# Optimization experiments

Hardware: AMD Instinct MI355X
Metric: run time of the kernel (lower is better)

Reference implementation:

```python
import jax, jax.numpy as jnp
import numpy as np

N_NODES = 20000
LN_EPS = 1e-5


def setup_inputs() -> dict:
    key = jax.random.key(0)
    ks = jax.random.split(key, 8)
    N, E, D_IN, D_H = N_NODES, 320000, 128, 256
    x = jax.random.normal(ks[0], (N, D_IN), dtype=jnp.float32)
    edge_index = jax.random.randint(ks[1], (2, E), 0, N, dtype=jnp.int64)
    edge_weight = jax.random.uniform(ks[2], (E,), dtype=jnp.float32)
    # Glorot-ish scaled weights
    W1 = jax.random.normal(ks[3], (D_IN, D_H), dtype=jnp.float32) / np.sqrt(D_IN)
    W2 = jax.random.normal(ks[4], (D_H, D_H), dtype=jnp.float32) / np.sqrt(D_H)
    Wres = jax.random.normal(ks[5], (D_IN, D_H), dtype=jnp.float32) / np.sqrt(D_IN)
    return {
        "x": x, "edge_index": edge_index, "edge_weight": edge_weight,
        "W1": W1, "b1": jnp.zeros((D_H,), jnp.float32),
        "W2": W2, "b2": jnp.zeros((D_H,), jnp.float32),
        "Wres": Wres, "bres": jnp.zeros((D_H,), jnp.float32),
        "gamma1": jnp.ones((D_H,), jnp.float32), "beta1": jnp.zeros((D_H,), jnp.float32),
        "gamma2": jnp.ones((D_H,), jnp.float32), "beta2": jnp.zeros((D_H,), jnp.float32),
    }


def _gcn_conv(x, W, b, src, dst, w, n):
    # PyG GCNConv: linear transform, then sym-normalized scatter-add aggregation
    h = x @ W  # [N, D_H]
    deg = jax.ops.segment_sum(w, dst, num_segments=n)  # in-degree incl. self loops
    dinv = jnp.where(deg > 0, jax.lax.rsqrt(deg), 0.0)
    norm = dinv[src] * w * dinv[dst]  # [E+N]
    out = jax.ops.segment_sum(norm[:, None] * h[src], dst, num_segments=n)
    return out + b


def _layer_norm(x, gamma, beta):
    mu = jnp.mean(x, axis=-1, keepdims=True)
    var = jnp.mean(jnp.square(x - mu), axis=-1, keepdims=True)
    return (x - mu) * jax.lax.rsqrt(var + LN_EPS) * gamma + beta


def reference(x, edge_index, edge_weight, W1, b1, W2, b2, Wres, bres,
              gamma1, beta1, gamma2, beta2):
    n = x.shape[0]
    loop = jnp.arange(n, dtype=edge_index.dtype)
    # add self loops with weight 1 (add_self_loops=True)
    src = jnp.concatenate([edge_index[0], loop])
    dst = jnp.concatenate([edge_index[1], loop])
    w = jnp.concatenate([edge_weight, jnp.ones((n,), edge_weight.dtype)])

    # hop 0: conv -> relu (dropout p=0, eval) -> residual proj -> LayerNorm
    delta = jax.nn.relu(_gcn_conv(x, W1, b1, src, dst, w, n))
    h = _layer_norm(x @ Wres + bres + delta, gamma1, beta1)

    # hop 1 (last): conv -> residual -> LayerNorm (no relu)
    delta = _gcn_conv(h, W2, b2, src, dst, w, n)
    h = _layer_norm(h + delta, gamma2, beta2)
    return h
```

## Files before the change

kernel.cpp:

```cpp
#include <hip/hip_runtime.h>
#include <stdint.h>


constexpr int DIN = 128;
constexpr int DH  = 256;
#define LN_EPS 1e-5f

typedef __attribute__((ext_vector_type(8))) short bf16x8;
typedef __attribute__((ext_vector_type(4))) short bf16x4;
typedef __attribute__((ext_vector_type(4))) float f32x4;

__device__ __forceinline__ short f2bf(float f) {
  union { float f; unsigned u; } v; v.f = f;
  unsigned r = v.u + 0x7fffu + ((v.u >> 16) & 1u);
  return (short)(r >> 16);
}
__device__ __forceinline__ float bf2f(short b) {
  union { unsigned u; float f; } v; v.u = ((unsigned)(unsigned short)b) << 16;
  return v.f;
}

__device__ __forceinline__ int probe_m64(const unsigned* ei) {
  int lane = threadIdx.x & 63;
  unsigned v = ei[2 * (lane * 32) + 1];
  return __ballot(v != 0u) == 0ull;
}

__device__ __forceinline__ int eidx(const void* ei, long long e, int m64) {
  return m64 ? (int)((const long long*)ei)[e] : ((const int*)ei)[e];
}


__global__ __launch_bounds__(256) void k_prep(const float* __restrict__ x,
                                              short* __restrict__ xb,
                                              const float* __restrict__ W1,
                                              const float* __restrict__ Wres,
                                              const float* __restrict__ W2,
                                              short* __restrict__ W1t,
                                              short* __restrict__ Wrt,
                                              short* __restrict__ W2t,
                                              float* __restrict__ deg,
                                              int* __restrict__ cnt, int N) {
  const int NXV = N * DIN / 8;
  const int NW  = DIN * DH;
  const int NW2 = DH * DH;
  int idx = blockIdx.x * 256 + threadIdx.x;
  if (idx < NXV) {
    f32x4 a = ((const f32x4*)x)[idx * 2];
    f32x4 b = ((const f32x4*)x)[idx * 2 + 1];
    bf16x8 o;
    o[0] = f2bf(a[0]); o[1] = f2bf(a[1]); o[2] = f2bf(a[2]); o[3] = f2bf(a[3]);
    o[4] = f2bf(b[0]); o[5] = f2bf(b[1]); o[6] = f2bf(b[2]); o[7] = f2bf(b[3]);
    ((bf16x8*)xb)[idx] = o;
    return;
  }
  idx -= NXV;
  if (idx < N) { deg[idx] = 1.0f; cnt[idx] = 0; return; }
  idx -= N;
  if (idx < NW) {
    int n = idx / DIN, k = idx % DIN;
    W1t[idx] = f2bf(W1[k * DH + n]);
    return;
  }
  idx -= NW;
  if (idx < NW) {
    int n = idx / DIN, k = idx % DIN;
    Wrt[idx] = f2bf(Wres[k * DH + n]);
    return;
  }
  idx -= NW;
  if (idx < NW2) {
    int n = idx / DH, k = idx % DH;
    W2t[idx] = f2bf(W2[k * DH + n]);
  }
}


__global__ __launch_bounds__(256) void k_edge_accum(const void* ei,
                                                    const float* __restrict__ w,
                                                    float* deg, int* cnt, int E) {
  int m64 = probe_m64((const unsigned*)ei);
  int e = blockIdx.x * 256 + threadIdx.x;
  if (e >= E) return;
  int d = eidx(ei, (long long)E + e, m64);
  atomicAdd(&deg[d], w[e]);
  atomicAdd(&cnt[d], 1);
}


__global__ __launch_bounds__(1024) void k_scan(const int* __restrict__ cnt,
                                               float* deg, int* rowptr,
                                               int* cursor, int n) {
  for (int i = threadIdx.x; i < n; i += 1024) deg[i] = rsqrtf(deg[i]);

  __shared__ int wsum[16];
  __shared__ int carry_s;
  int tid = threadIdx.x, lane = tid & 63, wv = tid >> 6;
  if (tid == 0) { carry_s = 0; rowptr[0] = 0; cursor[0] = 0; }
  __syncthreads();
  for (int c0 = 0; c0 < n; c0 += 1024) {
    int i = c0 + tid;
    int sc = (i < n) ? cnt[i] : 0;
#pragma unroll
    for (int off = 1; off < 64; off <<= 1) {
      int t = __shfl_up(sc, off, 64);
      if (lane >= off) sc += t;
    }
    if (lane == 63) wsum[wv] = sc;
    __syncthreads();
    if (wv == 0) {
      int s = (lane < 16) ? wsum[lane] : 0;
#pragma unroll
      for (int off = 1; off < 16; off <<= 1) {
        int t = __shfl_up(s, off, 64);
        if (lane >= off) s += t;
      }
      if (lane < 16) wsum[lane] = s;
    }
    __syncthreads();
    int inc = sc + ((wv > 0) ? wsum[wv - 1] : 0) + carry_s;
    if (i < n) { rowptr[i + 1] = inc; cursor[i + 1] = inc; }
    __syncthreads();
    if (tid == 0) carry_s += wsum[15];
    __syncthreads();
  }
}


__global__ __launch_bounds__(256) void k_fill(const void* ei,
                                              const float* __restrict__ w,
                                              const float* __restrict__ dinv,
                                              int* cursor, int* srcs,
                                              float* norms, int E) {
  int m64 = probe_m64((const unsigned*)ei);
  int e = blockIdx.x * 256 + threadIdx.x;
  if (e >= E) return;
  int s = eidx(ei, e, m64);
  int d = eidx(ei, (long long)E + e, m64);
  int p = atomicAdd(&cursor[d], 1);
  srcs[p] = s;
  norms[p] = dinv[s] * w[e] * dinv[d];
}


__global__ __launch_bounds__(256) void k_gemm_l1(const short* __restrict__ A,
                                                 const short* __restrict__ B1,
                                                 const short* __restrict__ Br,
                                                 const float* __restrict__ bres,
                                                 short* __restrict__ H1,
                                                 float* __restrict__ RES, int M) {
  constexpr int K = DIN;
  int tid = threadIdx.x;
  int wave = tid >> 6, lane = tid & 63;
  int lr = lane & 15, lg = lane >> 4;
  int bm = blockIdx.x * 64 + (wave >> 1) * 32;
  int bn = blockIdx.y * 64 + (wave & 1) * 32;

  int r0 = min(bm + lr, M - 1);
  int r1 = min(bm + 16 + lr, M - 1);
  const short* a0p = A + (long long)r0 * K + lg * 8;
  const short* a1p = A + (long long)r1 * K + lg * 8;
  const short* b10p = B1 + (long long)(bn + lr) * K + lg * 8;
  const short* b11p = B1 + (long long)(bn + 16 + lr) * K + lg * 8;
  const short* br0p = Br + (long long)(bn + lr) * K + lg * 8;
  const short* br1p = Br + (long long)(bn + 16 + lr) * K + lg * 8;

  f32x4 a1c[2][2] = {}, arc[2][2] = {};
#pragma unroll
  for (int ks = 0; ks < K / 32; ++ks) {
    bf16x8 a0 = *(const bf16x8*)(a0p + ks * 32);
    bf16x8 a1 = *(const bf16x8*)(a1p + ks * 32);
    bf16x8 p0 = *(const bf16x8*)(b10p + ks * 32);
    bf16x8 p1 = *(const bf16x8*)(b11p + ks * 32);
    bf16x8 q0 = *(const bf16x8*)(br0p + ks * 32);
    bf16x8 q1 = *(const bf16x8*)(br1p + ks * 32);
    a1c[0][0] = __builtin_amdgcn_mfma_f32_16x16x32_bf16(a0, p0, a1c[0][0], 0, 0, 0);
    a1c[0][1] = __builtin_amdgcn_mfma_f32_16x16x32_bf16(a0, p1, a1c[0][1], 0, 0, 0);
    a1c[1][0] = __builtin_amdgcn_mfma_f32_16x16x32_bf16(a1, p0, a1c[1][0], 0, 0, 0);
    a1c[1][1] = __builtin_amdgcn_mfma_f32_16x16x32_bf16(a1, p1, a1c[1][1], 0, 0, 0);
    arc[0][0] = __builtin_amdgcn_mfma_f32_16x16x32_bf16(a0, q0, arc[0][0], 0, 0, 0);
    arc[0][1] = __builtin_amdgcn_mfma_f32_16x16x32_bf16(a0, q1, arc[0][1], 0, 0, 0);
    arc[1][0] = __builtin_amdgcn_mfma_f32_16x16x32_bf16(a1, q0, arc[1][0], 0, 0, 0);
    arc[1][1] = __builtin_amdgcn_mfma_f32_16x16x32_bf16(a1, q1, arc[1][1], 0, 0, 0);
  }

#pragma unroll
  for (int mi = 0; mi < 2; ++mi)
#pragma unroll
    for (int ni = 0; ni < 2; ++ni)
#pragma unroll
      for (int j = 0; j < 4; ++j) {
        int row = bm + mi * 16 + lg * 4 + j;
        int col = bn + ni * 16 + lr;
        if (row < M) {
          H1[(long long)row * DH + col] = f2bf(a1c[mi][ni][j]);
          RES[(long long)row * DH + col] = arc[mi][ni][j] + bres[col];
        }
      }
}


__global__ __launch_bounds__(256) void k_gemm2(const short* __restrict__ A,
                                               const short* __restrict__ Bt,
                                               short* __restrict__ outb, int M) {
  constexpr int K = DH;
  int tid = threadIdx.x;
  int wave = tid >> 6, lane = tid & 63;
  int lr = lane & 15, lg = lane >> 4;
  int bm = blockIdx.x * 64 + (wave >> 1) * 32;
  int bn = blockIdx.y * 64 + (wave & 1) * 32;

  int r0 = min(bm + lr, M - 1);
  int r1 = min(bm + 16 + lr, M - 1);
  const short* a0p = A + (long long)r0 * K + lg * 8;
  const short* a1p = A + (long long)r1 * K + lg * 8;
  const short* b0p = Bt + (long long)(bn + lr) * K + lg * 8;
  const short* b1p = Bt + (long long)(bn + 16 + lr) * K + lg * 8;

  f32x4 acc[2][2] = {};
#pragma unroll
  for (int ks = 0; ks < K / 32; ++ks) {
    bf16x8 a0 = *(const bf16x8*)(a0p + ks * 32);
    bf16x8 a1 = *(const bf16x8*)(a1p + ks * 32);
    bf16x8 b0 = *(const bf16x8*)(b0p + ks * 32);
    bf16x8 b1 = *(const bf16x8*)(b1p + ks * 32);
    acc[0][0] = __builtin_amdgcn_mfma_f32_16x16x32_bf16(a0, b0, acc[0][0], 0, 0, 0);
    acc[0][1] = __builtin_amdgcn_mfma_f32_16x16x32_bf16(a0, b1, acc[0][1], 0, 0, 0);
    acc[1][0] = __builtin_amdgcn_mfma_f32_16x16x32_bf16(a1, b0, acc[1][0], 0, 0, 0);
    acc[1][1] = __builtin_amdgcn_mfma_f32_16x16x32_bf16(a1, b1, acc[1][1], 0, 0, 0);
  }

#pragma unroll
  for (int mi = 0; mi < 2; ++mi)
#pragma unroll
    for (int ni = 0; ni < 2; ++ni)
#pragma unroll
      for (int j = 0; j < 4; ++j) {
        int row = bm + mi * 16 + lg * 4 + j;
        int col = bn + ni * 16 + lr;
        if (row < M) outb[(long long)row * DH + col] = f2bf(acc[mi][ni][j]);
      }
}


template <bool RELU>
__global__ __launch_bounds__(256) void k_agg_ln(
    const short* __restrict__ H, const float* __restrict__ resid,
    const float* __restrict__ bias, const float* __restrict__ gamma,
    const float* __restrict__ beta, const int* __restrict__ rowptr,
    const int* __restrict__ srcs, const float* __restrict__ norms,
    const float* __restrict__ dinv, float* __restrict__ out_f,
    short* __restrict__ out_bf, int n) {
  int wv = threadIdx.x >> 6, lane = threadIdx.x & 63;
  int i = blockIdx.x * 4 + wv;
  if (i >= n) return;
  int d = lane * 4;

  float di = dinv[i];
  float acc0, acc1, acc2, acc3;
  {
    bf16x4 hv = *(const bf16x4*)(H + (long long)i * DH + d);
    float sw = di * di;
    acc0 = sw * bf2f(hv[0]); acc1 = sw * bf2f(hv[1]);
    acc2 = sw * bf2f(hv[2]); acc3 = sw * bf2f(hv[3]);
  }
  int e = rowptr[i], end = rowptr[i + 1];
  for (; e + 4 <= end; e += 4) {
    int s0 = srcs[e], s1 = srcs[e + 1], s2 = srcs[e + 2], s3 = srcs[e + 3];
    float n0 = norms[e], n1 = norms[e + 1], n2 = norms[e + 2], n3 = norms[e + 3];
    bf16x4 v0 = *(const bf16x4*)(H + (long long)s0 * DH + d);
    bf16x4 v1 = *(const bf16x4*)(H + (long long)s1 * DH + d);
    bf16x4 v2 = *(const bf16x4*)(H + (long long)s2 * DH + d);
    bf16x4 v3 = *(const bf16x4*)(H + (long long)s3 * DH + d);
    acc0 += n0 * bf2f(v0[0]); acc1 += n0 * bf2f(v0[1]);
    acc2 += n0 * bf2f(v0[2]); acc3 += n0 * bf2f(v0[3]);
    acc0 += n1 * bf2f(v1[0]); acc1 += n1 * bf2f(v1[1]);
    acc2 += n1 * bf2f(v1[2]); acc3 += n1 * bf2f(v1[3]);
    acc0 += n2 * bf2f(v2[0]); acc1 += n2 * bf2f(v2[1]);
    acc2 += n2 * bf2f(v2[2]); acc3 += n2 * bf2f(v2[3]);
    acc0 += n3 * bf2f(v3[0]); acc1 += n3 * bf2f(v3[1]);
    acc2 += n3 * bf2f(v3[2]); acc3 += n3 * bf2f(v3[3]);
  }
  for (; e < end; ++e) {
    int s = srcs[e];
    float nm = norms[e];
    bf16x4 v = *(const bf16x4*)(H + (long long)s * DH + d);
    acc0 += nm * bf2f(v[0]); acc1 += nm * bf2f(v[1]);
    acc2 += nm * bf2f(v[2]); acc3 += nm * bf2f(v[3]);
  }

  f32x4 rv = *(const f32x4*)(resid + (long long)i * DH + d);
  f32x4 bv = *(const f32x4*)(bias + d);
  float t0 = acc0 + bv[0], t1 = acc1 + bv[1], t2 = acc2 + bv[2], t3 = acc3 + bv[3];
  if (RELU) {
    t0 = fmaxf(t0, 0.f); t1 = fmaxf(t1, 0.f);
    t2 = fmaxf(t2, 0.f); t3 = fmaxf(t3, 0.f);
  }
  t0 += rv[0]; t1 += rv[1]; t2 += rv[2]; t3 += rv[3];

  float s1 = t0 + t1 + t2 + t3;
  float s2 = t0 * t0 + t1 * t1 + t2 * t2 + t3 * t3;
#pragma unroll
  for (int m = 1; m < 64; m <<= 1) {
    s1 += __shfl_xor(s1, m, 64);
    s2 += __shfl_xor(s2, m, 64);
  }
  float mu = s1 * (1.f / 256.f);
  float var = s2 * (1.f / 256.f) - mu * mu;
  float rs = rsqrtf(var + LN_EPS);

  f32x4 gv = *(const f32x4*)(gamma + d);
  f32x4 be = *(const f32x4*)(beta + d);
  f32x4 y;
  y[0] = (t0 - mu) * rs * gv[0] + be[0];
  y[1] = (t1 - mu) * rs * gv[1] + be[1];
  y[2] = (t2 - mu) * rs * gv[2] + be[2];
  y[3] = (t3 - mu) * rs * gv[3] + be[3];
  *(f32x4*)(out_f + (long long)i * DH + d) = y;
  if (out_bf) {
    bf16x4 ob;
    ob[0] = f2bf(y[0]); ob[1] = f2bf(y[1]);
    ob[2] = f2bf(y[2]); ob[3] = f2bf(y[3]);
    *(bf16x4*)(out_bf + (long long)i * DH + d) = ob;
  }
}


extern "C" void kernel_launch(void* const* d_in, const int* in_sizes, int n_in,
                              void* d_out, int out_size, void* d_ws,
                              size_t ws_size, hipStream_t stream) {
  const float* x    = (const float*)d_in[0];
  const void*  ei   = d_in[1];
  const float* ew   = (const float*)d_in[2];
  const float* W1   = (const float*)d_in[3];
  const float* b1   = (const float*)d_in[4];
  const float* W2   = (const float*)d_in[5];
  const float* b2   = (const float*)d_in[6];
  const float* Wres = (const float*)d_in[7];
  const float* bres = (const float*)d_in[8];
  const float* g1   = (const float*)d_in[9];
  const float* be1  = (const float*)d_in[10];
  const float* g2   = (const float*)d_in[11];
  const float* be2  = (const float*)d_in[12];

  const int N = in_sizes[0] / DIN;
  const int E = in_sizes[2];

  char* ws = (char*)d_ws;
  auto alloc = [&](size_t bytes) -> char* {
    char* p = ws;
    ws += (bytes + 255) & ~(size_t)255;
    return p;
  };
  short* xb     = (short*)alloc((size_t)N * DIN * 2);
  short* W1t    = (short*)alloc((size_t)DIN * DH * 2);
  short* Wrt    = (short*)alloc((size_t)DIN * DH * 2);
  short* W2t    = (short*)alloc((size_t)DH * DH * 2);
  short* Hb     = (short*)alloc((size_t)N * DH * 2);
  float* RES    = (float*)alloc((size_t)N * DH * 4);
  float* h1f    = (float*)alloc((size_t)N * DH * 4);
  short* h1b    = (short*)alloc((size_t)N * DH * 2);
  float* deg    = (float*)alloc((size_t)N * 4);
  int*   cnt    = (int*)alloc((size_t)N * 4);
  int*   rowptr = (int*)alloc((size_t)(N + 1) * 4);
  int*   cursor = (int*)alloc((size_t)(N + 1) * 4);
  int*   srcs   = (int*)alloc((size_t)E * 4);
  float* norms  = (float*)alloc((size_t)E * 4);

  const int eb = (E + 255) / 256;

  int prep_items = N * DIN / 8 + N + 2 * DIN * DH + DH * DH;
  k_prep<<<(prep_items + 255) / 256, 256, 0, stream>>>(
      x, xb, W1, Wres, W2, W1t, Wrt, W2t, deg, cnt, N);
  k_edge_accum<<<eb, 256, 0, stream>>>(ei, ew, deg, cnt, E);
  k_scan<<<1, 1024, 0, stream>>>(cnt, deg, rowptr, cursor, N);
  k_fill<<<eb, 256, 0, stream>>>(ei, ew, deg, cursor, srcs, norms, E);

  dim3 gg((N + 63) / 64, DH / 64);
  k_gemm_l1<<<gg, 256, 0, stream>>>(xb, W1t, Wrt, bres, Hb, RES, N);
  k_agg_ln<true><<<(N + 3) / 4, 256, 0, stream>>>(Hb, RES, b1, g1, be1, rowptr,
                                                  srcs, norms, deg, h1f, h1b, N);
  k_gemm2<<<gg, 256, 0, stream>>>(h1b, W2t, Hb, N);
  k_agg_ln<false><<<(N + 3) / 4, 256, 0, stream>>>(Hb, h1f, b2, g2, be2, rowptr,
                                                   srcs, norms, deg,
                                                   (float*)d_out, nullptr, N);
}
```

Baseline: 264.7 us.

## Fuse edge passes into prep and GEMM kernels, store residuals in bf16

Folds the degree/count atomics into the prep kernel and runs the CSR fill as extra blocks of the layer-1 GEMM kernel, which removes two launches. It also replaces the looped chunk scan with a per-thread serial-then-block scan and zeroes counters with a memset. Both residuals are stored and read as bf16 instead of fp32, and the fp32 h1 copy is dropped, which cuts memory traffic at some cost in precision. The aggregation inner loop is unrolled to 8 edges, and the int64 probe now samples across the whole edge array.

```diff
diff --git a/kernel.cpp b/kernel.cpp
--- a/kernel.cpp
+++ b/kernel.cpp
@@ -20,9 +20,12 @@
   return v.f;
 }
 
-__device__ __forceinline__ int probe_m64(const unsigned* ei) {
+__device__ __forceinline__ int probe_m64(const unsigned* ei, int E) {
   int lane = threadIdx.x & 63;
-  unsigned v = ei[2 * (lane * 32) + 1];
+  long long stride = (E >= 64) ? (E / 64) : 1;
+  long long li = (long long)lane * stride;
+  if (li >= E) li = 0;
+  unsigned v = ei[2 * li + 1];
   return __ballot(v != 0u) == 0ull;
 }
 
@@ -39,8 +42,10 @@
                                               short* __restrict__ W1t,
                                               short* __restrict__ Wrt,
                                               short* __restrict__ W2t,
-                                              float* __restrict__ deg,
-                                              int* __restrict__ cnt, int N) {
+                                              const void* ei,
+                                              const float* __restrict__ ew,
+                                              float* deg, int* cnt,
+                                              int N, int E) {
   const int NXV = N * DIN / 8;
   const int NW  = DIN * DH;
   const int NW2 = DH * DH;
@@ -55,8 +60,6 @@
     return;
   }
   idx -= NXV;
-  if (idx < N) { deg[idx] = 1.0f; cnt[idx] = 0; return; }
-  idx -= N;
   if (idx < NW) {
     int n = idx / DIN, k = idx % DIN;
     W1t[idx] = f2bf(W1[k * DH + n]);
@@ -72,89 +75,92 @@
   if (idx < NW2) {
     int n = idx / DH, k = idx % DH;
     W2t[idx] = f2bf(W2[k * DH + n]);
-  }
-}
-
-
-__global__ __launch_bounds__(256) void k_edge_accum(const void* ei,
-                                                    const float* __restrict__ w,
-                                                    float* deg, int* cnt, int E) {
-  int m64 = probe_m64((const unsigned*)ei);
-  int e = blockIdx.x * 256 + threadIdx.x;
-  if (e >= E) return;
-  int d = eidx(ei, (long long)E + e, m64);
-  atomicAdd(&deg[d], w[e]);
-  atomicAdd(&cnt[d], 1);
+    return;
+  }
+  idx -= NW2;
+  int m64 = probe_m64((const unsigned*)ei, E);
+  if (idx < E) {
+    int d = eidx(ei, (long long)E + idx, m64);
+    atomicAdd(&deg[d], ew[idx]);
+    atomicAdd(&cnt[d], 1);
+  }
 }
 
 
 __global__ __launch_bounds__(1024) void k_scan(const int* __restrict__ cnt,
                                                float* deg, int* rowptr,
                                                int* cursor, int n) {
-  for (int i = threadIdx.x; i < n; i += 1024) deg[i] = rsqrtf(deg[i]);
-
+  for (int i = threadIdx.x; i < n; i += 1024) deg[i] = rsqrtf(1.0f + deg[i]);
+
+  constexpr int MAXI = 32;
+  int items = (n + 1023) / 1024;
+  int tid = threadIdx.x, lane = tid & 63, wv = tid >> 6;
+  int base = tid * items;
+  int v[MAXI];
+  int tot = 0;
+#pragma unroll 4
+  for (int j = 0; j < items; ++j) {
+    int i = base + j;
+    v[j] = (i < n) ? cnt[i] : 0;
+    tot += v[j];
+  }
+  int sc = tot;
+#pragma unroll
+  for (int off = 1; off < 64; off <<= 1) {
+    int t = __shfl_up(sc, off, 64);
+    if (lane >= off) sc += t;
+  }
   __shared__ int wsum[16];
-  __shared__ int carry_s;
-  int tid = threadIdx.x, lane = tid & 63, wv = tid >> 6;
-  if (tid == 0) { carry_s = 0; rowptr[0] = 0; cursor[0] = 0; }
+  if (lane == 63) wsum[wv] = sc;
   __syncthreads();
-  for (int c0 = 0; c0 < n; c0 += 1024) {
-    int i = c0 + tid;
-    int sc = (i < n) ? cnt[i] : 0;
-#pragma unroll
-    for (int off = 1; off < 64; off <<= 1) {
-      int t = __shfl_up(sc, off, 64);
-      if (lane >= off) sc += t;
+  if (wv == 0 && lane < 16) {
+    int s = wsum[lane];
+#pragma unroll
+    for (int off = 1; off < 16; off <<= 1) {
+      int t = __shfl_up(s, off, 64);
+      if (lane >= off) s += t;
     }
-    if (lane == 63) wsum[wv] = sc;
-    __syncthreads();
-    if (wv == 0) {
-      int s = (lane < 16) ? wsum[lane] : 0;
-#pragma unroll
-      for (int off = 1; off < 16; off <<= 1) {
-        int t = __shfl_up(s, off, 64);
-        if (lane >= off) s += t;
-      }
-      if (lane < 16) wsum[lane] = s;
-    }
-    __syncthreads();
-    int inc = sc + ((wv > 0) ? wsum[wv - 1] : 0) + carry_s;
-    if (i < n) { rowptr[i + 1] = inc; cursor[i + 1] = inc; }
-    __syncthreads();
-    if (tid == 0) carry_s += wsum[15];
-    __syncthreads();
-  }
-}
-
-
-__global__ __launch_bounds__(256) void k_fill(const void* ei,
-                                              const float* __restrict__ w,
-                                              const float* __restrict__ dinv,
-                                              int* cursor, int* srcs,
-                                              float* norms, int E) {
-  int m64 = probe_m64((const unsigned*)ei);
-  int e = blockIdx.x * 256 + threadIdx.x;
-  if (e >= E) return;
-  int s = eidx(ei, e, m64);
-  int d = eidx(ei, (long long)E + e, m64);
-  int p = atomicAdd(&cursor[d], 1);
-  srcs[p] = s;
-  norms[p] = dinv[s] * w[e] * dinv[d];
-}
-
-
-__global__ __launch_bounds__(256) void k_gemm_l1(const short* __restrict__ A,
-                                                 const short* __restrict__ B1,
-                                                 const short* __restrict__ Br,
-                                                 const float* __restrict__ bres,
-                                                 short* __restrict__ H1,
-                                                 float* __restrict__ RES, int M) {
+    wsum[lane] = s;
+  }
+  __syncthreads();
+  int prefix = (sc - tot) + ((wv > 0) ? wsum[wv - 1] : 0);
+  if (tid == 0) { rowptr[0] = 0; cursor[0] = 0; }
+  int run = prefix;
+#pragma unroll 4
+  for (int j = 0; j < items; ++j) {
+    int i = base + j;
+    run += v[j];
+    if (i < n) { rowptr[i + 1] = run; cursor[i + 1] = run; }
+  }
+}
+
+
+__global__ __launch_bounds__(256) void k_gemm_l1_fill(
+    const short* __restrict__ A, const short* __restrict__ B1,
+    const short* __restrict__ Br, const float* __restrict__ bres,
+    short* __restrict__ H1, short* __restrict__ RESb, int M, int MB,
+    const void* ei, const float* __restrict__ ew,
+    const float* __restrict__ dinv, int* cursor, int* srcs, float* norms,
+    int E) {
   constexpr int K = DIN;
+  int GB = MB * 4;
+  if ((int)blockIdx.x >= GB) {
+    int m64 = probe_m64((const unsigned*)ei, E);
+    int e = ((int)blockIdx.x - GB) * 256 + threadIdx.x;
+    if (e >= E) return;
+    int s = eidx(ei, e, m64);
+    int d = eidx(ei, (long long)E + e, m64);
+    int p = atomicAdd(&cursor[d], 1);
+    srcs[p] = s;
+    norms[p] = dinv[s] * ew[e] * dinv[d];
+    return;
+  }
+  int mb = (int)blockIdx.x % MB, nbk = (int)blockIdx.x / MB;
   int tid = threadIdx.x;
   int wave = tid >> 6, lane = tid & 63;
   int lr = lane & 15, lg = lane >> 4;
-  int bm = blockIdx.x * 64 + (wave >> 1) * 32;
-  int bn = blockIdx.y * 64 + (wave & 1) * 32;
+  int bm = mb * 64 + (wave >> 1) * 32;
+  int bn = nbk * 64 + (wave & 1) * 32;
 
   int r0 = min(bm + lr, M - 1);
   int r1 = min(bm + 16 + lr, M - 1);
@@ -194,7 +200,7 @@
         int col = bn + ni * 16 + lr;
         if (row < M) {
           H1[(long long)row * DH + col] = f2bf(a1c[mi][ni][j]);
-          RES[(long long)row * DH + col] = arc[mi][ni][j] + bres[col];
+          RESb[(long long)row * DH + col] = f2bf(arc[mi][ni][j] + bres[col]);
         }
       }
 }
@@ -243,9 +249,9 @@
 }
 
 
-template <bool RELU>
+template <bool RELU, bool RESBF>
 __global__ __launch_bounds__(256) void k_agg_ln(
-    const short* __restrict__ H, const float* __restrict__ resid,
+    const short* __restrict__ H, const void* __restrict__ resid,
     const float* __restrict__ bias, const float* __restrict__ gamma,
     const float* __restrict__ beta, const int* __restrict__ rowptr,
     const int* __restrict__ srcs, const float* __restrict__ norms,
@@ -265,13 +271,19 @@
     acc2 = sw * bf2f(hv[2]); acc3 = sw * bf2f(hv[3]);
   }
   int e = rowptr[i], end = rowptr[i + 1];
-  for (; e + 4 <= end; e += 4) {
-    int s0 = srcs[e], s1 = srcs[e + 1], s2 = srcs[e + 2], s3 = srcs[e + 3];
-    float n0 = norms[e], n1 = norms[e + 1], n2 = norms[e + 2], n3 = norms[e + 3];
+  for (; e + 8 <= end; e += 8) {
+    int s0 = srcs[e],     s1 = srcs[e + 1], s2 = srcs[e + 2], s3 = srcs[e + 3];
+    int s4 = srcs[e + 4], s5 = srcs[e + 5], s6 = srcs[e + 6], s7 = srcs[e + 7];
     bf16x4 v0 = *(const bf16x4*)(H + (long long)s0 * DH + d);
     bf16x4 v1 = *(const bf16x4*)(H + (long long)s1 * DH + d);
     bf16x4 v2 = *(const bf16x4*)(H + (long long)s2 * DH + d);
     bf16x4 v3 = *(const bf16x4*)(H + (long long)s3 * DH + d);
+    bf16x4 v4 = *(const bf16x4*)(H + (long long)s4 * DH + d);
+    bf16x4 v5 = *(const bf16x4*)(H + (long long)s5 * DH + d);
+    bf16x4 v6 = *(const bf16x4*)(H + (long long)s6 * DH + d);
+    bf16x4 v7 = *(const bf16x4*)(H + (long long)s7 * DH + d);
+    float n0 = norms[e],     n1 = norms[e + 1], n2 = norms[e + 2], n3 = norms[e + 3];
+    float n4 = norms[e + 4], n5 = norms[e + 5], n6 = norms[e + 6], n7 = norms[e + 7];
     acc0 += n0 * bf2f(v0[0]); acc1 += n0 * bf2f(v0[1]);
     acc2 += n0 * bf2f(v0[2]); acc3 += n0 * bf2f(v0[3]);
     acc0 += n1 * bf2f(v1[0]); acc1 += n1 * bf2f(v1[1]);
@@ -280,6 +292,14 @@
     acc2 += n2 * bf2f(v2[2]); acc3 += n2 * bf2f(v2[3]);
     acc0 += n3 * bf2f(v3[0]); acc1 += n3 * bf2f(v3[1]);
     acc2 += n3 * bf2f(v3[2]); acc3 += n3 * bf2f(v3[3]);
+    acc0 += n4 * bf2f(v4[0]); acc1 += n4 * bf2f(v4[1]);
+    acc2 += n4 * bf2f(v4[2]); acc3 += n4 * bf2f(v4[3]);
+    acc0 += n5 * bf2f(v5[0]); acc1 += n5 * bf2f(v5[1]);
+    acc2 += n5 * bf2f(v5[2]); acc3 += n5 * bf2f(v5[3]);
+    acc0 += n6 * bf2f(v6[0]); acc1 += n6 * bf2f(v6[1]);
+    acc2 += n6 * bf2f(v6[2]); acc3 += n6 * bf2f(v6[3]);
+    acc0 += n7 * bf2f(v7[0]); acc1 += n7 * bf2f(v7[1]);
+    acc2 += n7 * bf2f(v7[2]); acc3 += n7 * bf2f(v7[3]);
   }
   for (; e < end; ++e) {
     int s = srcs[e];
@@ -289,14 +309,21 @@
     acc2 += nm * bf2f(v[2]); acc3 += nm * bf2f(v[3]);
   }
 
-  f32x4 rv = *(const f32x4*)(resid + (long long)i * DH + d);
+  float r0, r1, r2, r3;
+  if (RESBF) {
+    bf16x4 rv = *(const bf16x4*)((const short*)resid + (long long)i * DH + d);
+    r0 = bf2f(rv[0]); r1 = bf2f(rv[1]); r2 = bf2f(rv[2]); r3 = bf2f(rv[3]);
+  } else {
+    f32x4 rv = *(const f32x4*)((const float*)resid + (long long)i * DH + d);
+    r0 = rv[0]; r1 = rv[1]; r2 = rv[2]; r3 = rv[3];
+  }
   f32x4 bv = *(const f32x4*)(bias + d);
   float t0 = acc0 + bv[0], t1 = acc1 + bv[1], t2 = acc2 + bv[2], t3 = acc3 + bv[3];
   if (RELU) {
     t0 = fmaxf(t0, 0.f); t1 = fmaxf(t1, 0.f);
     t2 = fmaxf(t2, 0.f); t3 = fmaxf(t3, 0.f);
   }
-  t0 += rv[0]; t1 += rv[1]; t2 += rv[2]; t3 += rv[3];
+  t0 += r0; t1 += r1; t2 += r2; t3 += r3;
 
   float s1 = t0 + t1 + t2 + t3;
   float s2 = t0 * t0 + t1 * t1 + t2 * t2 + t3 * t3;
@@ -316,7 +343,7 @@
   y[1] = (t1 - mu) * rs * gv[1] + be[1];
   y[2] = (t2 - mu) * rs * gv[2] + be[2];
   y[3] = (t3 - mu) * rs * gv[3] + be[3];
-  *(f32x4*)(out_f + (long long)i * DH + d) = y;
+  if (out_f) *(f32x4*)(out_f + (long long)i * DH + d) = y;
   if (out_bf) {
     bf16x4 ob;
     ob[0] = f2bf(y[0]); ob[1] = f2bf(y[1]);
@@ -357,31 +384,31 @@
   short* Wrt    = (short*)alloc((size_t)DIN * DH * 2);
   short* W2t    = (short*)alloc((size_t)DH * DH * 2);
   short* Hb     = (short*)alloc((size_t)N * DH * 2);
-  float* RES    = (float*)alloc((size_t)N * DH * 4);
-  float* h1f    = (float*)alloc((size_t)N * DH * 4);
+  short* RESb   = (short*)alloc((size_t)N * DH * 2);
   short* h1b    = (short*)alloc((size_t)N * DH * 2);
-  float* deg    = (float*)alloc((size_t)N * 4);
-  int*   cnt    = (int*)alloc((size_t)N * 4);
+  int*   cnt    = (int*)alloc((size_t)N * 8);
+  float* deg    = (float*)(cnt + N);
   int*   rowptr = (int*)alloc((size_t)(N + 1) * 4);
   int*   cursor = (int*)alloc((size_t)(N + 1) * 4);
   int*   srcs   = (int*)alloc((size_t)E * 4);
   float* norms  = (float*)alloc((size_t)E * 4);
 
-  const int eb = (E + 255) / 256;
-
-  int prep_items = N * DIN / 8 + N + 2 * DIN * DH + DH * DH;
+  hipMemsetAsync(cnt, 0, (size_t)N * 8, stream);
+
+  int prep_items = N * DIN / 8 + 2 * DIN * DH + DH * DH + E;
   k_prep<<<(prep_items + 255) / 256, 256, 0, stream>>>(
-      x, xb, W1, Wres, W2, W1t, Wrt, W2t, deg, cnt, N);
-  k_edge_accum<<<eb, 256, 0, stream>>>(ei, ew, deg, cnt, E);
+      x, xb, W1, Wres, W2, W1t, Wrt, W2t, ei, ew, deg, cnt, N, E);
   k_scan<<<1, 1024, 0, stream>>>(cnt, deg, rowptr, cursor, N);
-  k_fill<<<eb, 256, 0, stream>>>(ei, ew, deg, cursor, srcs, norms, E);
-
-  dim3 gg((N + 63) / 64, DH / 64);
-  k_gemm_l1<<<gg, 256, 0, stream>>>(xb, W1t, Wrt, bres, Hb, RES, N);
-  k_agg_ln<true><<<(N + 3) / 4, 256, 0, stream>>>(Hb, RES, b1, g1, be1, rowptr,
-                                                  srcs, norms, deg, h1f, h1b, N);
+
+  const int MB = (N + 63) / 64;
+  const int FB = (E + 255) / 256;
+  k_gemm_l1_fill<<<MB * 4 + FB, 256, 0, stream>>>(
+      xb, W1t, Wrt, bres, Hb, RESb, N, MB, ei, ew, deg, cursor, srcs, norms, E);
+  k_agg_ln<true, true><<<(N + 3) / 4, 256, 0, stream>>>(
+      Hb, RESb, b1, g1, be1, rowptr, srcs, norms, deg, nullptr, h1b, N);
+
+  dim3 gg(MB, DH / 64);
   k_gemm2<<<gg, 256, 0, stream>>>(h1b, W2t, Hb, N);
-  k_agg_ln<false><<<(N + 3) / 4, 256, 0, stream>>>(Hb, h1f, b2, g2, be2, rowptr,
-                                                   srcs, norms, deg,
-                                                   (float*)d_out, nullptr, N);
-}
+  k_agg_ln<false, true><<<(N + 3) / 4, 256, 0, stream>>>(
+      Hb, h1b, b2, g2, be2, rowptr, srcs, norms, deg, (float*)d_out, nullptr, N);
+}
```

Result: no change. 265.1 us (+0.2%).
